# Kernel optimization log

Hardware: AMD Instinct MI355X
Metric: run time of the kernel (lower is better)

## Reference

```python
import jax, jax.numpy as jnp
import numpy as np

N = 4096        # nodes
E = 131072      # edges (avg degree 32)
IN = 512        # in_channels
HID = 512       # hidden_channels
HEADS = 4       # GAT heads
LAYERS = 3      # residual GCN layers
G = 16          # graphs in batch
OUT = 1         # out_channels
NEG_SLOPE = 0.2 # GAT LeakyReLU slope


def setup_inputs() -> dict:
    key = jax.random.key(0)
    ks = jax.random.split(key, 9)
    s = 0.02
    x = jax.random.normal(ks[0], (N, IN), dtype=jnp.float32)
    edge_index = jax.random.randint(ks[1], (2, E), 0, N)
    batch = jnp.sort(jax.random.randint(ks[2], (N,), 0, G))
    W_gat = jax.random.normal(ks[3], (HEADS, IN, HID), dtype=jnp.float32) * s
    a_src = jax.random.normal(ks[4], (HEADS, HID), dtype=jnp.float32) * s
    a_dst = jax.random.normal(ks[5], (HEADS, HID), dtype=jnp.float32) * s
    W_gcn = jax.random.normal(ks[6], (LAYERS, HID, HID), dtype=jnp.float32) * s
    fc_w = jax.random.normal(ks[7], (HID, OUT), dtype=jnp.float32) * s
    fc_b = jnp.zeros((OUT,), dtype=jnp.float32)
    return {"x": x, "edge_index": edge_index, "batch": batch,
            "W_gat": W_gat, "a_src": a_src, "a_dst": a_dst,
            "W_gcn": W_gcn, "fc_w": fc_w, "fc_b": fc_b}


def reference(x, edge_index, batch, W_gat, a_src, a_dst, W_gcn, fc_w, fc_b):
    src, dst = edge_index[0], edge_index[1]

    # ---- LatentRelationCapturerGAT: multi-head GAT, one output per head ----
    h = jnp.einsum('nc,hcd->nhd', x, W_gat)                    # [N,H,D]
    lg_src = jnp.einsum('nhd,hd->nh', h, a_src)                # [N,H]
    lg_dst = jnp.einsum('nhd,hd->nh', h, a_dst)                # [N,H]
    e = jax.nn.leaky_relu(lg_src[src] + lg_dst[dst], NEG_SLOPE)  # [E,H]
    # segment softmax over incoming edges of each destination node
    m = jax.ops.segment_max(e, dst, num_segments=N)            # [N,H]
    w = jnp.exp(e - m[dst])                                    # [E,H]
    z = jax.ops.segment_sum(w, dst, num_segments=N)            # [N,H]
    alpha = w / (z[dst] + 1e-16)                               # [E,H]
    H0 = jax.ops.segment_sum(alpha[:, :, None] * h[src], dst, num_segments=N)  # [N,H,D]

    # ---- dense adjacency build + GCN normalization (shared across heads) ----
    A = jnp.zeros((N, N), dtype=x.dtype).at[src, dst].set(1.0)
    A = A + jnp.eye(N, dtype=x.dtype)                          # self-loops
    dinv = jax.lax.rsqrt(jnp.sum(A, axis=1))                   # deg >= 1
    A_hat = dinv[:, None] * A * dinv[None, :]                  # D^-1/2 (A+I) D^-1/2

    # ---- DeepResidualGCN: H <- relu(A_hat @ H @ W_l) + H (heads batched) ----
    H = H0
    for l in range(W_gcn.shape[0]):
        P = jnp.einsum('nm,mhd->nhd', A_hat, H)                # propagate
        H = jax.nn.relu(jnp.einsum('nhd,de->nhe', P, W_gcn[l])) + H

    # ---- per-head global mean pool, then mean over heads ----
    ones = jnp.ones((N,), dtype=x.dtype)
    cnt = jnp.maximum(jax.ops.segment_sum(ones, batch, num_segments=G), 1.0)  # [G]
    pooled = jax.ops.segment_sum(H, batch, num_segments=G) / cnt[:, None, None]  # [G,H,D]
    feats = pooled.mean(axis=1)                                # [G,D]

    return feats @ fc_w + fc_b                                 # [G,OUT]
```

## Files before the change

### kernel.cpp

```cpp
#include <hip/hip_runtime.h>
#include <cstdint>
#include <cstddef>

#define Nn    4096
#define Ee    131072
#define INC   512
#define HIDC  512
#define HEADS 4
#define NLAY  3
#define GG    16
#define FW    2048
#define LDA   40

typedef __attribute__((ext_vector_type(8))) short bfrag;
typedef __attribute__((ext_vector_type(4))) float ffrag;

__device__ __forceinline__ ushort f2bf(float v){
  uint u = __builtin_bit_cast(uint, v);
  u += 0x7fffu + ((u>>16)&1u);
  return (ushort)(u>>16);
}
__device__ __forceinline__ float bf2f(ushort s){
  uint u = ((uint)s)<<16; return __builtin_bit_cast(float, u);
}
__device__ __forceinline__ void fma8(float* acc, uint4 g, float w){
  uint u[4] = {g.x, g.y, g.z, g.w};
  #pragma unroll
  for (int q=0;q<4;q++){
    float lo = __builtin_bit_cast(float, u[q]<<16);
    float hi = __builtin_bit_cast(float, u[q] & 0xffff0000u);
    acc[2*q]   += w*lo;
    acc[2*q+1] += w*hi;
  }
}
__device__ __forceinline__ uint4 pack8(const float* a){
  uint4 o;
  o.x = (uint)f2bf(a[0]) | ((uint)f2bf(a[1])<<16);
  o.y = (uint)f2bf(a[2]) | ((uint)f2bf(a[3])<<16);
  o.z = (uint)f2bf(a[4]) | ((uint)f2bf(a[5])<<16);
  o.w = (uint)f2bf(a[6]) | ((uint)f2bf(a[7])<<16);
  return o;
}

__global__ __launch_bounds__(256) void tobf(const float* __restrict__ X, ushort* __restrict__ Xb){
  int i = blockIdx.x*256 + threadIdx.x;
  Xb[i] = f2bf(X[i]);
}

__global__ __launch_bounds__(256) void tbf(const float* __restrict__ W, ushort* __restrict__ T){
  __shared__ float tile[32][33];
  int b = blockIdx.z;
  int r0 = blockIdx.y*32, c0 = blockIdx.x*32;
  int t = threadIdx.x;
  int i = t>>3, j0 = (t&7)*4;
  const float* Wb = W + (size_t)b*512*512;
  float4 v = *(const float4*)(Wb + (size_t)(r0+i)*512 + c0 + j0);
  tile[i][j0]=v.x; tile[i][j0+1]=v.y; tile[i][j0+2]=v.z; tile[i][j0+3]=v.w;
  __syncthreads();
  ushort* o = T + (size_t)b*512*512 + (size_t)(c0+i)*512 + r0 + j0;
  #pragma unroll
  for (int q=0;q<4;q++) o[q] = f2bf(tile[j0+q][i]);
}

__global__ __launch_bounds__(256) void gemm_bf(
    const ushort* __restrict__ A, const ushort* __restrict__ B,
    const float* __restrict__ Res, float* __restrict__ Cf, ushort* __restrict__ Cb,
    int M, int N, int K, int relu_res)
{
  __shared__ __align__(16) ushort Ah[128*LDA];
  __shared__ __align__(16) ushort Bh[128*LDA];
  int t = threadIdx.x;
  int m0 = blockIdx.y*128, n0 = blockIdx.x*128;
  int srow = t>>1, scol = (t&1)*16;
  int wave = t>>6, lane = t&63;
  int wm = (wave&1)*64, wn = (wave>>1)*64;
  int lm = lane&15, quad = lane>>4;

  ffrag acc[4][4];
  #pragma unroll
  for (int i=0;i<4;i++){
    #pragma unroll
    for (int j=0;j<4;j++) acc[i][j] = (ffrag){0.f,0.f,0.f,0.f};
  }

  const ushort* pA = A + (size_t)(m0+srow)*K + scol;
  const ushort* pB = B + (size_t)(n0+srow)*K + scol;

  uint4 ra0 = *(const uint4*)(pA);  uint4 ra1 = *(const uint4*)(pA+8);
  uint4 rb0 = *(const uint4*)(pB);  uint4 rb1 = *(const uint4*)(pB+8);

  int sidx = srow*LDA + scol;
  for (int k0 = 0; k0 < K; k0 += 32){
    __syncthreads();
    *(uint4*)&Ah[sidx] = ra0; *(uint4*)&Ah[sidx+8] = ra1;
    *(uint4*)&Bh[sidx] = rb0; *(uint4*)&Bh[sidx+8] = rb1;
    __syncthreads();
    if (k0+32 < K){
      ra0 = *(const uint4*)(pA+k0+32); ra1 = *(const uint4*)(pA+k0+40);
      rb0 = *(const uint4*)(pB+k0+32); rb1 = *(const uint4*)(pB+k0+40);
    }
    bfrag af[4];
    #pragma unroll
    for (int mt=0; mt<4; mt++)
      af[mt] = *(const bfrag*)&Ah[(wm+mt*16+lm)*LDA + quad*8];
    #pragma unroll
    for (int nt=0; nt<4; nt++){
      bfrag bf = *(const bfrag*)&Bh[(wn+nt*16+lm)*LDA + quad*8];
      #pragma unroll
      for (int mt=0; mt<4; mt++)
        acc[mt][nt] = __builtin_amdgcn_mfma_f32_16x16x32_bf16(af[mt], bf, acc[mt][nt], 0,0,0);
    }
  }

  #pragma unroll
  for (int mt=0; mt<4; mt++){
    #pragma unroll
    for (int nt=0; nt<4; nt++){
      #pragma unroll
      for (int r=0;r<4;r++){
        int grow = m0 + wm + mt*16 + quad*4 + r;
        int gcol = n0 + wn + nt*16 + lm;
        size_t off = (size_t)grow*N + gcol;
        float v = acc[mt][nt][r];
        if (relu_res) v = fmaxf(v,0.f) + Res[off];
        if (Cf) Cf[off] = v;
        if (Cb) Cb[off] = f2bf(v);
      }
    }
  }
}

__global__ __launch_bounds__(256) void compute_lg(const ushort* __restrict__ hbf,
    const float* __restrict__ a_src, const float* __restrict__ a_dst,
    float* __restrict__ lgs, float* __restrict__ lgd){
  int n = blockIdx.x; int t = threadIdx.x;
  int hd = t>>6, lane = t&63;
  uint4 g = *(const uint4*)(hbf + (size_t)n*FW + hd*HIDC + lane*8);
  float h[8] = {0,0,0,0,0,0,0,0};
  fma8(h, g, 1.0f);
  float4 as0 = *(const float4*)(a_src + hd*HIDC + lane*8);
  float4 as1 = *(const float4*)(a_src + hd*HIDC + lane*8 + 4);
  float4 ad0 = *(const float4*)(a_dst + hd*HIDC + lane*8);
  float4 ad1 = *(const float4*)(a_dst + hd*HIDC + lane*8 + 4);
  float s1 = h[0]*as0.x + h[1]*as0.y + h[2]*as0.z + h[3]*as0.w
           + h[4]*as1.x + h[5]*as1.y + h[6]*as1.z + h[7]*as1.w;
  float s2 = h[0]*ad0.x + h[1]*ad0.y + h[2]*ad0.z + h[3]*ad0.w
           + h[4]*ad1.x + h[5]*ad1.y + h[6]*ad1.z + h[7]*ad1.w;
  for (int off=32; off; off>>=1){ s1 += __shfl_down(s1,off); s2 += __shfl_down(s2,off); }
  if (lane==0){ lgs[n*HEADS+hd]=s1; lgd[n*HEADS+hd]=s2; }
}

__global__ __launch_bounds__(256) void hist_dst(const int* __restrict__ dst, int* __restrict__ indeg){
  int e = blockIdx.x*256+threadIdx.x; if (e<Ee) atomicAdd(&indeg[dst[e]],1);
}
__global__ __launch_bounds__(1024) void exscan(const int* __restrict__ cnt, int* __restrict__ rowptr, int n){
  __shared__ int sums[1024];
  int t = threadIdx.x;
  int v[4]; int s=0;
  #pragma unroll
  for (int i=0;i<4;i++){ int idx=t*4+i; v[i] = (idx<n)? cnt[idx] : 0; s+=v[i]; }
  sums[t]=s; __syncthreads();
  for (int off=1; off<1024; off<<=1){
    int other = (t>=off)? sums[t-off] : 0;
    __syncthreads();
    sums[t] += other;
    __syncthreads();
  }
  int run = (t>0)? sums[t-1] : 0;
  #pragma unroll
  for (int i=0;i<4;i++){ int idx=t*4+i; if (idx<n) rowptr[idx]=run; run+=v[i]; }
  if (t==1023) rowptr[n]=sums[1023];
}
__global__ __launch_bounds__(256) void scatter_dst(const int* __restrict__ src, const int* __restrict__ dst,
    const int* __restrict__ rowptr, int* __restrict__ fill, int* __restrict__ slist){
  int e = blockIdx.x*256+threadIdx.x; if (e>=Ee) return;
  int d = dst[e]; int p = atomicAdd(&fill[d],1); slist[rowptr[d]+p]=src[e];
}
__global__ __launch_bounds__(256) void dedup_mark(const int* __restrict__ src, const int* __restrict__ dst,
    unsigned int* __restrict__ bitmap, int* __restrict__ cnt, int* __restrict__ flag){
  int e = blockIdx.x*256+threadIdx.x; if (e>=Ee) return;
  unsigned int key = (unsigned int)src[e]*Nn + (unsigned int)dst[e];
  unsigned int bit = 1u<<(key&31);
  unsigned int old = atomicOr(&bitmap[key>>5], bit);
  if (!(old & bit)){ flag[e]=1; atomicAdd(&cnt[src[e]],1); }
}
__global__ __launch_bounds__(256) void scatter_src(const int* __restrict__ src, const int* __restrict__ dst,
    const int* __restrict__ flag, const int* __restrict__ rowptr, int* __restrict__ fill, int* __restrict__ cols){
  int e = blockIdx.x*256+threadIdx.x; if (e>=Ee) return;
  if (!flag[e]) return;
  int s = src[e]; int p = atomicAdd(&fill[s],1); cols[rowptr[s]+p] = dst[e];
}
__global__ __launch_bounds__(256) void compute_dinv(const int* __restrict__ cnt, float* __restrict__ dinv){
  int n = blockIdx.x*256+threadIdx.x; if (n<Nn) dinv[n] = 1.0f/sqrtf((float)(1+cnt[n]));
}

__global__ __launch_bounds__(256) void gat_aggregate(const ushort* __restrict__ hbf,
    const float* __restrict__ lgs, const float* __restrict__ lgd,
    const int* __restrict__ rowptr, const int* __restrict__ slist,
    float* __restrict__ Hfeat, ushort* __restrict__ Hbf){
  int t = threadIdx.x;
  int wv = __builtin_amdgcn_readfirstlane(t>>6);
  int lane = t&63;
  int b = blockIdx.x;
  int hd = __builtin_amdgcn_readfirstlane(b & 3);
  int n = ((b>>2)<<2) + wv;
  int beg = rowptr[n], deg = rowptr[n+1]-beg;
  float ldst = lgd[n*HEADS+hd];
  float m_ = -3.4e38f, z_ = 0.f;
  int   s0 = 0; float v0 = 0.f;
  for (int i=lane; i<deg; i+=64){
    int s = slist[beg+i];
    float v = lgs[s*HEADS+hd] + ldst;
    v = v>0.f ? v : 0.2f*v;
    if (i<64){ s0=s; v0=v; }
    float mn = fmaxf(m_, v);
    z_ = z_*__expf(m_-mn) + __expf(v-mn);
    m_ = mn;
  }
  for (int o=32;o;o>>=1){
    float mo = __shfl_down(m_,o), zo = __shfl_down(z_,o);
    float mn = fmaxf(m_, mo);
    z_ = z_*__expf(m_-mn) + zo*__expf(mo-mn);
    m_ = mn;
  }
  float mx = __shfl(m_,0);
  float zs = __shfl(z_,0);
  float inv = 1.f/(zs+1e-16f);
  float acc[8] = {0,0,0,0,0,0,0,0};
  const ushort* hb = hbf + hd*HIDC + lane*8;
  for (int base=0; base<deg; base+=64){
    float al; int s;
    if (base==0){
      s = s0;
      al = (lane<deg) ? __expf(v0-mx)*inv : 0.f;
    } else {
      int i = base+lane;
      al = 0.f; s = 0;
      if (i<deg){
        s = slist[beg+i];
        float v = lgs[s*HEADS+hd] + ldst; v = v>0.f ? v : 0.2f*v;
        al = __expf(v-mx)*inv;
      }
    }
    int cn = min(64, deg-base);
    int c = 0;
    for (; c+4<=cn; c+=4){
      float a0=__shfl(al,c),   a1=__shfl(al,c+1), a2=__shfl(al,c+2), a3=__shfl(al,c+3);
      int   s0_=__shfl(s,c),   s1_=__shfl(s,c+1), s2_=__shfl(s,c+2), s3_=__shfl(s,c+3);
      uint4 g0 = *(const uint4*)(hb + (size_t)s0_*FW);
      uint4 g1 = *(const uint4*)(hb + (size_t)s1_*FW);
      uint4 g2 = *(const uint4*)(hb + (size_t)s2_*FW);
      uint4 g3 = *(const uint4*)(hb + (size_t)s3_*FW);
      fma8(acc, g0, a0); fma8(acc, g1, a1); fma8(acc, g2, a2); fma8(acc, g3, a3);
    }
    for (; c<cn; c++){
      float a = __shfl(al,c);
      int ss  = __shfl(s,c);
      uint4 g = *(const uint4*)(hb + (size_t)ss*FW);
      fma8(acc, g, a);
    }
  }
  size_t off = (size_t)n*FW + hd*HIDC + lane*8;
  *(float4*)(Hfeat + off)     = make_float4(acc[0],acc[1],acc[2],acc[3]);
  *(float4*)(Hfeat + off + 4) = make_float4(acc[4],acc[5],acc[6],acc[7]);
  *(uint4*)(Hbf + off) = pack8(acc);
}

__global__ __launch_bounds__(256) void spmm_bf(const ushort* __restrict__ Hbf,
    ushort* __restrict__ Phi,
    const int* __restrict__ rowptr, const int* __restrict__ cols, const float* __restrict__ dinv){
  int t = threadIdx.x;
  int wv = __builtin_amdgcn_readfirstlane(t>>6);
  int lane = t&63;
  int b = blockIdx.x;
  int ck = __builtin_amdgcn_readfirstlane(b & 3);
  int n = ((b>>2)<<2) + wv;
  int f = (ck<<9) + lane*8;
  float di = dinv[n];
  float acc[8] = {0,0,0,0,0,0,0,0};
  const ushort* hb = Hbf + f;
  uint4 self = *(const uint4*)(hb + (size_t)n*FW);
  fma8(acc, self, di*di);
  int beg = rowptr[n], end = rowptr[n+1];
  for (int base=beg; base<end; base+=64){
    int i = base + lane;
    int m = n; float w = 0.f;
    if (i < end){ m = cols[i]; w = di*dinv[m]; }
    int cn = min(64, end-base);
    int c = 0;
    for (; c+4<=cn; c+=4){
      int   m0=__shfl(m,c),   m1=__shfl(m,c+1), m2=__shfl(m,c+2), m3=__shfl(m,c+3);
      float w0=__shfl(w,c),   w1=__shfl(w,c+1), w2=__shfl(w,c+2), w3=__shfl(w,c+3);
      uint4 g0 = *(const uint4*)(hb + (size_t)m0*FW);
      uint4 g1 = *(const uint4*)(hb + (size_t)m1*FW);
      uint4 g2 = *(const uint4*)(hb + (size_t)m2*FW);
      uint4 g3 = *(const uint4*)(hb + (size_t)m3*FW);
      fma8(acc, g0, w0); fma8(acc, g1, w1); fma8(acc, g2, w2); fma8(acc, g3, w3);
    }
    for (; c<cn; c++){
      int mm   = __shfl(m,c);
      float ww = __shfl(w,c);
      uint4 g = *(const uint4*)(hb + (size_t)mm*FW);
      fma8(acc, g, ww);
    }
  }
  *(uint4*)(Phi + (size_t)n*FW + f) = pack8(acc);
}

__global__ __launch_bounds__(256) void graph_offsets(const int* __restrict__ batch, int* __restrict__ goff){
  __shared__ int cnt[GG];
  int t = threadIdx.x;
  if (t<GG) cnt[t]=0;
  __syncthreads();
  for (int i=t;i<Nn;i+=256) atomicAdd(&cnt[batch[i]],1);
  __syncthreads();
  if (t==0){ int run=0; for (int g=0; g<GG; g++){ goff[g]=run; run+=cnt[g]; } goff[GG]=run; }
}
__global__ __launch_bounds__(256) void pool_accum(const float* __restrict__ H,
    const int* __restrict__ batch, float* __restrict__ psum){
  int d = blockIdx.y*256 + threadIdx.x;
  int n0 = blockIdx.x*32;
  int g = batch[n0];
  float s = 0.f;
  for (int k=0;k<32;k++){
    int n = n0+k;
    int gn = batch[n];
    if (gn != g){ atomicAdd(&psum[(size_t)g*FW+d], s); s=0.f; g=gn; }
    s += H[(size_t)n*FW + d];
  }
  atomicAdd(&psum[(size_t)g*FW+d], s);
}
__global__ __launch_bounds__(256) void final_out(const float* __restrict__ psum,
    const int* __restrict__ goff,
    const float* __restrict__ fc_w, const float* __restrict__ fc_b, float* __restrict__ out){
  int g = blockIdx.x; int t = threadIdx.x;
  float cinv = 0.25f / fmaxf((float)(goff[g+1]-goff[g]), 1.f);
  float p = 0.f;
  for (int d=t; d<HIDC; d+=256){
    float f = cinv*(psum[(size_t)g*FW+d] + psum[(size_t)g*FW+HIDC+d]
                  + psum[(size_t)g*FW+2*HIDC+d] + psum[(size_t)g*FW+3*HIDC+d]);
    p += f*fc_w[d];
  }
  __shared__ float red[4];
  for (int off=32; off; off>>=1) p += __shfl_down(p,off);
  if ((t&63)==0) red[t>>6]=p;
  __syncthreads();
  if (t==0) out[g] = red[0]+red[1]+red[2]+red[3] + fc_b[0];
}

extern "C" void kernel_launch(void* const* d_in, const int* in_sizes, int n_in,
                              void* d_out, int out_size, void* d_ws, size_t ws_size,
                              hipStream_t stream){
  const float* x      = (const float*)d_in[0];
  const int*   ei     = (const int*)d_in[1];
  const int*   batch  = (const int*)d_in[2];
  const float* W_gat  = (const float*)d_in[3];
  const float* a_src  = (const float*)d_in[4];
  const float* a_dst  = (const float*)d_in[5];
  const float* W_gcn  = (const float*)d_in[6];
  const float* fc_w   = (const float*)d_in[7];
  const float* fc_b   = (const float*)d_in[8];
  float* out = (float*)d_out;
  const int* src = ei;
  const int* dst = ei + Ee;

  char* w = (char*)d_ws;
  size_t off = 0;
  auto alloc = [&](size_t bytes)->char*{ char* p = w + off; off = (off + bytes + 255) & ~(size_t)255; return p; };
  float*  Hfeat  = (float*)alloc((size_t)Nn*FW*4);
  ushort* hbf    = (ushort*)alloc((size_t)Nn*FW*2);
  ushort* Hbf    = (ushort*)alloc((size_t)Nn*FW*2);
  ushort* Xbf    = (ushort*)alloc((size_t)Nn*INC*2);
  ushort* WgatT  = (ushort*)alloc((size_t)HEADS*INC*HIDC*2);
  ushort* WgcnT  = (ushort*)alloc((size_t)NLAY*HIDC*HIDC*2);
  float* lgs    = (float*)alloc((size_t)Nn*HEADS*4);
  float* lgd    = (float*)alloc((size_t)Nn*HEADS*4);
  int* indeg    = (int*)alloc(Nn*4);
  int* rowptr_d = (int*)alloc((Nn+1)*4);
  int* slist    = (int*)alloc(Ee*4);
  int* fill_d   = (int*)alloc(Nn*4);
  unsigned int* bitmap = (unsigned int*)alloc((size_t)Nn*Nn/8);
  int* cnt_s    = (int*)alloc(Nn*4);
  int* rowptr_s = (int*)alloc((Nn+1)*4);
  int* cols     = (int*)alloc(Ee*4);
  int* fill_s   = (int*)alloc(Nn*4);
  int* flag     = (int*)alloc(Ee*4);
  float* dinv   = (float*)alloc(Nn*4);
  float* psum   = (float*)alloc((size_t)GG*FW*4);
  int* goff     = (int*)alloc((GG+1)*4);
  ushort* Phi   = hbf;

  hipMemsetAsync(indeg, 0, Nn*4, stream);
  hipMemsetAsync(fill_d, 0, Nn*4, stream);
  hipMemsetAsync(cnt_s, 0, Nn*4, stream);
  hipMemsetAsync(fill_s, 0, Nn*4, stream);
  hipMemsetAsync(flag, 0, Ee*4, stream);
  hipMemsetAsync(bitmap, 0, (size_t)Nn*Nn/8, stream);
  hipMemsetAsync(psum, 0, (size_t)GG*FW*4, stream);

  tobf<<<(Nn*INC)/256,256,0,stream>>>(x, Xbf);
  tbf<<<dim3(16,16,HEADS),256,0,stream>>>(W_gat, WgatT);
  tbf<<<dim3(16,16,NLAY),256,0,stream>>>(W_gcn, WgcnT);

  gemm_bf<<<dim3(FW/128, Nn/128),256,0,stream>>>(Xbf, WgatT,
      nullptr, nullptr, hbf, Nn, FW, INC, 0);
  compute_lg<<<Nn,256,0,stream>>>(hbf, a_src, a_dst, lgs, lgd);

  hist_dst<<<Ee/256,256,0,stream>>>(dst, indeg);
  exscan<<<1,1024,0,stream>>>(indeg, rowptr_d, Nn);
  scatter_dst<<<Ee/256,256,0,stream>>>(src, dst, rowptr_d, fill_d, slist);
  gat_aggregate<<<Nn,256,0,stream>>>(hbf, lgs, lgd, rowptr_d, slist, Hfeat, Hbf);

  dedup_mark<<<Ee/256,256,0,stream>>>(src, dst, bitmap, cnt_s, flag);
  exscan<<<1,1024,0,stream>>>(cnt_s, rowptr_s, Nn);
  scatter_src<<<Ee/256,256,0,stream>>>(src, dst, flag, rowptr_s, fill_s, cols);
  compute_dinv<<<Nn/256,256,0,stream>>>(cnt_s, dinv);

  for (int l=0;l<NLAY;l++){
    spmm_bf<<<Nn,256,0,stream>>>(Hbf, Phi, rowptr_s, cols, dinv);
    gemm_bf<<<dim3(HIDC/128, (Nn*HEADS)/128),256,0,stream>>>(Phi,
        WgcnT + (size_t)l*HIDC*HIDC,
        Hfeat, Hfeat, (l==NLAY-1)? nullptr : Hbf, Nn*HEADS, HIDC, HIDC, 1);
  }

  graph_offsets<<<1,256,0,stream>>>(batch, goff);
  pool_accum<<<dim3(Nn/32, FW/256),256,0,stream>>>(Hfeat, batch, psum);
  final_out<<<GG,256,0,stream>>>(psum, goff, fc_w, fc_b, out);
}
```

Baseline: 424.8 us.

## Fuse graph-build edge passes, prepack column weights, and relayout GEMM LDS tiles

```diff
diff --git a/kernel.cpp b/kernel.cpp
--- a/kernel.cpp
+++ b/kernel.cpp
@@ -10,7 +10,6 @@
 #define NLAY  3
 #define GG    16
 #define FW    2048
-#define LDA   40
 
 typedef __attribute__((ext_vector_type(8))) short bfrag;
 typedef __attribute__((ext_vector_type(4))) float ffrag;
@@ -67,11 +66,11 @@
     const float* __restrict__ Res, float* __restrict__ Cf, ushort* __restrict__ Cb,
     int M, int N, int K, int relu_res)
 {
-  __shared__ __align__(16) ushort Ah[128*LDA];
-  __shared__ __align__(16) ushort Bh[128*LDA];
+  __shared__ __align__(16) ushort Ah[4096];
+  __shared__ __align__(16) ushort Bh[4096];
   int t = threadIdx.x;
   int m0 = blockIdx.y*128, n0 = blockIdx.x*128;
-  int srow = t>>1, scol = (t&1)*16;
+  int srow = t>>1, c = t&1, scol = c*16;
   int wave = t>>6, lane = t&63;
   int wm = (wave&1)*64, wn = (wave>>1)*64;
   int lm = lane&15, quad = lane>>4;
@@ -89,11 +88,12 @@
   uint4 ra0 = *(const uint4*)(pA);  uint4 ra1 = *(const uint4*)(pA+8);
   uint4 rb0 = *(const uint4*)(pB);  uint4 rb1 = *(const uint4*)(pB+8);
 
-  int sidx = srow*LDA + scol;
+  int w0 = ((2*c)*128 + srow)*8;
+  int w1 = w0 + 1024;
   for (int k0 = 0; k0 < K; k0 += 32){
     __syncthreads();
-    *(uint4*)&Ah[sidx] = ra0; *(uint4*)&Ah[sidx+8] = ra1;
-    *(uint4*)&Bh[sidx] = rb0; *(uint4*)&Bh[sidx+8] = rb1;
+    *(uint4*)&Ah[w0] = ra0; *(uint4*)&Ah[w1] = ra1;
+    *(uint4*)&Bh[w0] = rb0; *(uint4*)&Bh[w1] = rb1;
     __syncthreads();
     if (k0+32 < K){
       ra0 = *(const uint4*)(pA+k0+32); ra1 = *(const uint4*)(pA+k0+40);
@@ -102,10 +102,10 @@
     bfrag af[4];
     #pragma unroll
     for (int mt=0; mt<4; mt++)
-      af[mt] = *(const bfrag*)&Ah[(wm+mt*16+lm)*LDA + quad*8];
+      af[mt] = *(const bfrag*)&Ah[(quad*128 + wm + mt*16 + lm)*8];
     #pragma unroll
     for (int nt=0; nt<4; nt++){
-      bfrag bf = *(const bfrag*)&Bh[(wn+nt*16+lm)*LDA + quad*8];
+      bfrag bf = *(const bfrag*)&Bh[(quad*128 + wn + nt*16 + lm)*8];
       #pragma unroll
       for (int mt=0; mt<4; mt++)
         acc[mt][nt] = __builtin_amdgcn_mfma_f32_16x16x32_bf16(af[mt], bf, acc[mt][nt], 0,0,0);
@@ -150,15 +150,29 @@
   if (lane==0){ lgs[n*HEADS+hd]=s1; lgd[n*HEADS+hd]=s2; }
 }
 
-__global__ __launch_bounds__(256) void hist_dst(const int* __restrict__ dst, int* __restrict__ indeg){
-  int e = blockIdx.x*256+threadIdx.x; if (e<Ee) atomicAdd(&indeg[dst[e]],1);
-}
-__global__ __launch_bounds__(1024) void exscan(const int* __restrict__ cnt, int* __restrict__ rowptr, int n){
+__global__ __launch_bounds__(256) void edge_pass1(const int* __restrict__ src, const int* __restrict__ dst,
+    int* __restrict__ indeg, unsigned int* __restrict__ bitmap,
+    int* __restrict__ cnt_s, int* __restrict__ flag){
+  int e = blockIdx.x*256+threadIdx.x; if (e>=Ee) return;
+  int s = src[e], d = dst[e];
+  atomicAdd(&indeg[d],1);
+  unsigned int key = (unsigned int)s*Nn + (unsigned int)d;
+  unsigned int bit = 1u<<(key&31);
+  unsigned int old = atomicOr(&bitmap[key>>5], bit);
+  int f = (old & bit) ? 0 : 1;
+  flag[e] = f;
+  if (f) atomicAdd(&cnt_s[s],1);
+}
+
+__global__ __launch_bounds__(1024) void exscan2(const int* __restrict__ cnt0, int* __restrict__ rp0,
+    const int* __restrict__ cnt1, int* __restrict__ rp1){
+  const int* cnt = blockIdx.x ? cnt1 : cnt0;
+  int* rowptr    = blockIdx.x ? rp1  : rp0;
   __shared__ int sums[1024];
   int t = threadIdx.x;
   int v[4]; int s=0;
   #pragma unroll
-  for (int i=0;i<4;i++){ int idx=t*4+i; v[i] = (idx<n)? cnt[idx] : 0; s+=v[i]; }
+  for (int i=0;i<4;i++){ int idx=t*4+i; v[i] = cnt[idx]; s+=v[i]; }
   sums[t]=s; __syncthreads();
   for (int off=1; off<1024; off<<=1){
     int other = (t>=off)? sums[t-off] : 0;
@@ -168,30 +182,26 @@
   }
   int run = (t>0)? sums[t-1] : 0;
   #pragma unroll
-  for (int i=0;i<4;i++){ int idx=t*4+i; if (idx<n) rowptr[idx]=run; run+=v[i]; }
-  if (t==1023) rowptr[n]=sums[1023];
-}
-__global__ __launch_bounds__(256) void scatter_dst(const int* __restrict__ src, const int* __restrict__ dst,
-    const int* __restrict__ rowptr, int* __restrict__ fill, int* __restrict__ slist){
-  int e = blockIdx.x*256+threadIdx.x; if (e>=Ee) return;
-  int d = dst[e]; int p = atomicAdd(&fill[d],1); slist[rowptr[d]+p]=src[e];
-}
-__global__ __launch_bounds__(256) void dedup_mark(const int* __restrict__ src, const int* __restrict__ dst,
-    unsigned int* __restrict__ bitmap, int* __restrict__ cnt, int* __restrict__ flag){
-  int e = blockIdx.x*256+threadIdx.x; if (e>=Ee) return;
-  unsigned int key = (unsigned int)src[e]*Nn + (unsigned int)dst[e];
-  unsigned int bit = 1u<<(key&31);
-  unsigned int old = atomicOr(&bitmap[key>>5], bit);
-  if (!(old & bit)){ flag[e]=1; atomicAdd(&cnt[src[e]],1); }
-}
-__global__ __launch_bounds__(256) void scatter_src(const int* __restrict__ src, const int* __restrict__ dst,
-    const int* __restrict__ flag, const int* __restrict__ rowptr, int* __restrict__ fill, int* __restrict__ cols){
-  int e = blockIdx.x*256+threadIdx.x; if (e>=Ee) return;
-  if (!flag[e]) return;
-  int s = src[e]; int p = atomicAdd(&fill[s],1); cols[rowptr[s]+p] = dst[e];
-}
+  for (int i=0;i<4;i++){ int idx=t*4+i; rowptr[idx]=run; run+=v[i]; }
+  if (t==1023) rowptr[Nn]=sums[1023];
+}
+
 __global__ __launch_bounds__(256) void compute_dinv(const int* __restrict__ cnt, float* __restrict__ dinv){
   int n = blockIdx.x*256+threadIdx.x; if (n<Nn) dinv[n] = 1.0f/sqrtf((float)(1+cnt[n]));
+}
+
+__global__ __launch_bounds__(256) void edge_pass2(const int* __restrict__ src, const int* __restrict__ dst,
+    const int* __restrict__ flag,
+    const int* __restrict__ rp_d, int* __restrict__ fill_d, int* __restrict__ slist,
+    const int* __restrict__ rp_s, int* __restrict__ fill_s, int2* __restrict__ cw,
+    const float* __restrict__ dinv){
+  int e = blockIdx.x*256+threadIdx.x; if (e>=Ee) return;
+  int s = src[e], d = dst[e];
+  int p = atomicAdd(&fill_d[d],1); slist[rp_d[d]+p] = s;
+  if (flag[e]){
+    int q = atomicAdd(&fill_s[s],1);
+    cw[rp_s[s]+q] = make_int2(d, __float_as_int(dinv[d]));
+  }
 }
 
 __global__ __launch_bounds__(256) void gat_aggregate(const ushort* __restrict__ hbf,
@@ -268,7 +278,7 @@
 
 __global__ __launch_bounds__(256) void spmm_bf(const ushort* __restrict__ Hbf,
     ushort* __restrict__ Phi,
-    const int* __restrict__ rowptr, const int* __restrict__ cols, const float* __restrict__ dinv){
+    const int* __restrict__ rowptr, const int2* __restrict__ cw, const float* __restrict__ dinv){
   int t = threadIdx.x;
   int wv = __builtin_amdgcn_readfirstlane(t>>6);
   int lane = t&63;
@@ -285,7 +295,7 @@
   for (int base=beg; base<end; base+=64){
     int i = base + lane;
     int m = n; float w = 0.f;
-    if (i < end){ m = cols[i]; w = di*dinv[m]; }
+    if (i < end){ int2 e = cw[i]; m = e.x; w = di*__int_as_float(e.y); }
     int cn = min(64, end-base);
     int c = 0;
     for (; c+4<=cn; c+=4){
@@ -382,7 +392,7 @@
   unsigned int* bitmap = (unsigned int*)alloc((size_t)Nn*Nn/8);
   int* cnt_s    = (int*)alloc(Nn*4);
   int* rowptr_s = (int*)alloc((Nn+1)*4);
-  int* cols     = (int*)alloc(Ee*4);
+  int2* cwlist  = (int2*)alloc((size_t)Ee*8);
   int* fill_s   = (int*)alloc(Nn*4);
   int* flag     = (int*)alloc(Ee*4);
   float* dinv   = (float*)alloc(Nn*4);
@@ -394,7 +404,6 @@
   hipMemsetAsync(fill_d, 0, Nn*4, stream);
   hipMemsetAsync(cnt_s, 0, Nn*4, stream);
   hipMemsetAsync(fill_s, 0, Nn*4, stream);
-  hipMemsetAsync(flag, 0, Ee*4, stream);
   hipMemsetAsync(bitmap, 0, (size_t)Nn*Nn/8, stream);
   hipMemsetAsync(psum, 0, (size_t)GG*FW*4, stream);
 
@@ -406,18 +415,15 @@
       nullptr, nullptr, hbf, Nn, FW, INC, 0);
   compute_lg<<<Nn,256,0,stream>>>(hbf, a_src, a_dst, lgs, lgd);
 
-  hist_dst<<<Ee/256,256,0,stream>>>(dst, indeg);
-  exscan<<<1,1024,0,stream>>>(indeg, rowptr_d, Nn);
-  scatter_dst<<<Ee/256,256,0,stream>>>(src, dst, rowptr_d, fill_d, slist);
+  edge_pass1<<<Ee/256,256,0,stream>>>(src, dst, indeg, bitmap, cnt_s, flag);
+  exscan2<<<2,1024,0,stream>>>(indeg, rowptr_d, cnt_s, rowptr_s);
+  compute_dinv<<<Nn/256,256,0,stream>>>(cnt_s, dinv);
+  edge_pass2<<<Ee/256,256,0,stream>>>(src, dst, flag, rowptr_d, fill_d, slist,
+                                      rowptr_s, fill_s, cwlist, dinv);
   gat_aggregate<<<Nn,256,0,stream>>>(hbf, lgs, lgd, rowptr_d, slist, Hfeat, Hbf);
 
-  dedup_mark<<<Ee/256,256,0,stream>>>(src, dst, bitmap, cnt_s, flag);
-  exscan<<<1,1024,0,stream>>>(cnt_s, rowptr_s, Nn);
-  scatter_src<<<Ee/256,256,0,stream>>>(src, dst, flag, rowptr_s, fill_s, cols);
-  compute_dinv<<<Nn/256,256,0,stream>>>(cnt_s, dinv);
-
   for (int l=0;l<NLAY;l++){
-    spmm_bf<<<Nn,256,0,stream>>>(Hbf, Phi, rowptr_s, cols, dinv);
+    spmm_bf<<<Nn,256,0,stream>>>(Hbf, Phi, rowptr_s, cwlist, dinv);
     gemm_bf<<<dim3(HIDC/128, (Nn*HEADS)/128),256,0,stream>>>(Phi,
         WgcnT + (size_t)l*HIDC*HIDC,
         Hfeat, Hfeat, (l==NLAY-1)? nullptr : Hbf, Nn*HEADS, HIDC, HIDC, 1);
```

New measurement: 407.6 us. 4.1% less time.
